# Optimization experiments

Hardware: AMD Instinct MI355X
Metric: run time of the kernel (lower is better)

Reference implementation:

```python
import jax, jax.numpy as jnp
import numpy as np

N_NODES = 50000
N_EDGES = 800000
D_IN = 128
HIDDEN = 128
N_CLASSES = 10
N_GRAPHS = 128


def setup_inputs() -> dict:
    key = jax.random.key(0)
    ks = jax.random.split(key, 16)
    x = jax.random.normal(ks[0], (N_NODES, D_IN), dtype=jnp.float32)
    edge_index = jax.random.randint(ks[1], (2, N_EDGES), 0, N_NODES, dtype=jnp.int64)
    batch = jnp.sort(jax.random.randint(ks[2], (N_NODES,), 0, N_GRAPHS, dtype=jnp.int64))

    def lin(k, fin, fout):
        return jax.random.normal(k, (fin, fout), dtype=jnp.float32) / np.sqrt(fin)

    inp = {"x": x, "edge_index": edge_index, "batch": batch}
    # SAGEConv layer 1: in=D_IN, out=HIDDEN; layers 2,3: HIDDEN->HIDDEN
    dims = [(D_IN, HIDDEN), (HIDDEN, HIDDEN), (HIDDEN, HIDDEN)]
    for i, (fin, fout) in enumerate(dims, start=1):
        inp[f"Wl{i}"] = lin(ks[2 + 2 * i], fin, fout)       # neighbor transform
        inp[f"bl{i}"] = jnp.zeros((fout,), dtype=jnp.float32)
        inp[f"Wr{i}"] = lin(ks[3 + 2 * i], fin, fout)       # root transform
    inp["W1"] = lin(ks[12], HIDDEN, HIDDEN)
    inp["b1"] = jnp.zeros((HIDDEN,), dtype=jnp.float32)
    inp["W2"] = lin(ks[13], HIDDEN, N_CLASSES)
    inp["b2"] = jnp.zeros((N_CLASSES,), dtype=jnp.float32)
    return inp


def _sage_conv(x, src, dst, Wl, bl, Wr):
    # mean-aggregate neighbor features then linear; plus root linear (PyG SAGEConv)
    msg = x[src]                                               # [E, d] gather
    agg = jax.ops.segment_sum(msg, dst, num_segments=N_NODES)  # [N, d]
    cnt = jax.ops.segment_sum(jnp.ones_like(dst, dtype=x.dtype), dst,
                              num_segments=N_NODES)
    agg = agg / jnp.maximum(cnt, 1.0)[:, None]
    return agg @ Wl + bl + x @ Wr


def reference(x, edge_index, batch, Wl1, bl1, Wr1, Wl2, bl2, Wr2,
              Wl3, bl3, Wr3, W1, b1, W2, b2):
    src, dst = edge_index[0], edge_index[1]
    h = jax.nn.relu(_sage_conv(x, src, dst, Wl1, bl1, Wr1))
    h = jax.nn.relu(_sage_conv(h, src, dst, Wl2, bl2, Wr2))
    h = jax.nn.relu(_sage_conv(h, src, dst, Wl3, bl3, Wr3))
    # global_mean_pool over graph ids
    gsum = jax.ops.segment_sum(h, batch, num_segments=N_GRAPHS)
    gcnt = jax.ops.segment_sum(jnp.ones((h.shape[0],), h.dtype), batch,
                               num_segments=N_GRAPHS)
    g = gsum / jnp.maximum(gcnt, 1.0)[:, None]                 # [G, hidden]
    g = jax.nn.relu(g @ W1 + b1)
    # dropout is identity at inference (training=False)
    logits = g @ W2 + b2
    return jax.nn.log_softmax(logits, axis=-1)
```

## Files before the change

### kernel.cpp

```cpp
#include <hip/hip_runtime.h>

#define NN 50000
#define NE 800000
#define D 128
#define NG 128
#define NGRP 8
#define GRPSZ 6250
#define FILL_NB 392
#define ESL ((NE + 48) / 49)
#define CAP 64

typedef __attribute__((ext_vector_type(8))) short bf16x8;
typedef __attribute__((ext_vector_type(4))) float f32x4;

static __device__ __forceinline__ ushort f2bf(float f) {
    uint x = __float_as_uint(f);
    x += 0x7fffu + ((x >> 16) & 1u);
    return (ushort)(x >> 16);
}
static __device__ __forceinline__ float bf2f(ushort u) { return __uint_as_float((uint)u << 16); }
static __device__ __forceinline__ float blo16(uint u) { return __uint_as_float(u << 16); }
static __device__ __forceinline__ float bhi16(uint u) { return __uint_as_float(u & 0xffff0000u); }

#define CASTX_NB 6250
#define CASTW_NB 192
__global__ __launch_bounds__(256) void fusedA_kernel(
    const float* __restrict__ x, ushort* __restrict__ xb,
    const float* __restrict__ Wl1, const float* __restrict__ Wr1,
    const float* __restrict__ Wl2, const float* __restrict__ Wr2,
    const float* __restrict__ Wl3, const float* __restrict__ Wr3,
    ushort* __restrict__ wlh, ushort* __restrict__ wll,
    ushort* __restrict__ wrh, ushort* __restrict__ wrl) {
    const int bid = blockIdx.x;
    if (bid < CASTX_NB) {
        int i = bid * 256 + threadIdx.x;
        int n = i >> 5, g = i & 31;
        float4 v = *reinterpret_cast<const float4*>(x + (size_t)n * D + g * 4);
        ushort4 o;
        o.x = f2bf(v.x); o.y = f2bf(v.y); o.z = f2bf(v.z); o.w = f2bf(v.w);
        *reinterpret_cast<ushort4*>(xb + (size_t)n * D + g * 4) = o;
    } else {
        int i = (bid - CASTX_NB) * 256 + threadIdx.x;
        int layer = i >> 14, j = i & 16383;
        int colg = j >> 7, k = j & 127;
        const float* Wl = (layer == 0) ? Wl1 : ((layer == 1) ? Wl2 : Wl3);
        const float* Wr = (layer == 0) ? Wr1 : ((layer == 1) ? Wr2 : Wr3);
        float vl = Wl[k * 128 + colg];
        float vr = Wr[k * 128 + colg];
        ushort hl = f2bf(vl), hr = f2bf(vr);
        wlh[i] = hl; wll[i] = f2bf(vl - bf2f(hl));
        wrh[i] = hr; wrl[i] = f2bf(vr - bf2f(hr));
    }
}

static __device__ __forceinline__ void gemm2_body(
    char* As, int rb,
    const ushort* __restrict__ ain,
    const ushort* __restrict__ wlh, const ushort* __restrict__ wll,
    const ushort* __restrict__ wrh, const ushort* __restrict__ wrl,
    const float* __restrict__ bl,
    ushort* __restrict__ y, ushort* __restrict__ z, int N) {
    const int tid = threadIdx.x;
    const int w = tid >> 6, lane = tid & 63;
    const int row0 = rb * 128;
    const int lrow = lane & 15, lk = lane >> 4;
    const int colg = w * 16 + lrow;

    bf16x8 ylh[4], yll[4], zrh[4], zrl[4];
#pragma unroll
    for (int kb = 0; kb < 4; ++kb) {
        int off = colg * 128 + kb * 32 + lk * 8;
        ylh[kb] = *reinterpret_cast<const bf16x8*>(wlh + off);
        yll[kb] = *reinterpret_cast<const bf16x8*>(wll + off);
        zrh[kb] = *reinterpret_cast<const bf16x8*>(wrh + off);
        zrl[kb] = *reinterpret_cast<const bf16x8*>(wrl + off);
    }
    const float bias = bl[colg];

    {
        const char* gbase = (const char*)ain + (size_t)row0 * 256;
#pragma unroll
        for (int i = 0; i < 4; ++i) {
            int Ld = i * 8192 + w * 1024 + lane * 16;
            int gs = Ld ^ (((Ld >> 8) & 7) << 4);
            __builtin_amdgcn_global_load_lds(
                (const uint*)(gbase + gs),
                (uint*)(As + i * 8192 + w * 1024), 16, 0, 0);
        }
    }
    __syncthreads();

#pragma unroll
    for (int mt = 0; mt < 8; ++mt) {
        const int ar = mt * 16 + lrow;
        const int swz = (ar & 7) << 4;
        const char* ap = As + ar * 256;
        bf16x8 ah[4];
#pragma unroll
        for (int kb = 0; kb < 4; ++kb) {
            int b_ = kb * 64 + lk * 16;
            ah[kb] = *reinterpret_cast<const bf16x8*>(ap + (b_ ^ swz));
        }
        f32x4 accy = {0.f, 0.f, 0.f, 0.f}, accz = {0.f, 0.f, 0.f, 0.f};
#pragma unroll
        for (int kb = 0; kb < 4; ++kb) {
            accy = __builtin_amdgcn_mfma_f32_16x16x32_bf16(ah[kb], ylh[kb], accy, 0, 0, 0);
            accy = __builtin_amdgcn_mfma_f32_16x16x32_bf16(ah[kb], yll[kb], accy, 0, 0, 0);
            accz = __builtin_amdgcn_mfma_f32_16x16x32_bf16(ah[kb], zrh[kb], accz, 0, 0, 0);
            accz = __builtin_amdgcn_mfma_f32_16x16x32_bf16(ah[kb], zrl[kb], accz, 0, 0, 0);
        }
#pragma unroll
        for (int r = 0; r < 4; ++r) {
            int rowg = row0 + mt * 16 + lk * 4 + r;
            if (rowg < N) {
                y[(size_t)rowg * D + colg] = f2bf(accy[r]);
                z[(size_t)rowg * D + colg] = f2bf(accz[r] + bias);
            }
        }
    }
}

__global__ __launch_bounds__(512, 4) void gemm2_kernel(
    const ushort* __restrict__ ain,
    const ushort* __restrict__ wlh, const ushort* __restrict__ wll,
    const ushort* __restrict__ wrh, const ushort* __restrict__ wrl,
    const float* __restrict__ bl,
    ushort* __restrict__ y, ushort* __restrict__ z, int N) {
    __shared__ char As[128 * 256];
    gemm2_body(As, blockIdx.x, ain, wlh, wll, wrh, wrl, bl, y, z, N);
}

#define GEMM_NB 391
__global__ __launch_bounds__(512, 4) void fusedB_kernel(
    const ushort* __restrict__ ain,
    const ushort* __restrict__ wlh, const ushort* __restrict__ wll,
    const ushort* __restrict__ wrh, const ushort* __restrict__ wrl,
    const float* __restrict__ bl,
    ushort* __restrict__ y, ushort* __restrict__ z,
    const int* __restrict__ src, const int* __restrict__ dst,
    int* __restrict__ fillp, int* __restrict__ col, int N) {
    __shared__ char As[128 * 256];
    const int bid = blockIdx.x;
    if (bid < FILL_NB) {
        const int grp = bid & 7;
        const int slice = bid >> 3;
        const int dlo = grp * GRPSZ, dhi = dlo + GRPSZ;
        const int e0 = slice * ESL;
        const int e1 = min(e0 + ESL, NE);
        for (int e = e0 + (int)threadIdx.x; e < e1; e += 512) {
            int d = dst[e];
            if (d >= dlo && d < dhi) {
                int s = src[e];
                int pos = atomicAdd(&fillp[d], 1);
                if (pos < CAP) col[d * CAP + pos] = s;
            }
        }
    } else {
        gemm2_body(As, bid - FILL_NB, ain, wlh, wll, wrh, wrl, bl, y, z, N);
    }
}

__global__ __launch_bounds__(256) void gather_relu(
    const ushort* __restrict__ y, ushort* __restrict__ z,
    const int* __restrict__ deg, const int* __restrict__ col, int N) {
    int wid = (blockIdx.x * 256 + threadIdx.x) >> 6;
    if (wid >= N) return;
    const int lane = threadIdx.x & 63;
    const int h = lane >> 5, li = lane & 31;
    const int dg = deg[wid];
    const int lo = wid * CAP;
    const int hi = lo + min(dg, CAP);
    float a0 = 0.f, a1 = 0.f, a2 = 0.f, a3 = 0.f;
    int e = lo + h;
    for (; e + 6 < hi; e += 8) {
        int s0 = col[e], s1 = col[e + 2], s2 = col[e + 4], s3 = col[e + 6];
        uint2 v0 = *reinterpret_cast<const uint2*>(y + (size_t)s0 * D + li * 4);
        uint2 v1 = *reinterpret_cast<const uint2*>(y + (size_t)s1 * D + li * 4);
        uint2 v2 = *reinterpret_cast<const uint2*>(y + (size_t)s2 * D + li * 4);
        uint2 v3 = *reinterpret_cast<const uint2*>(y + (size_t)s3 * D + li * 4);
        a0 += (blo16(v0.x) + blo16(v1.x)) + (blo16(v2.x) + blo16(v3.x));
        a1 += (bhi16(v0.x) + bhi16(v1.x)) + (bhi16(v2.x) + bhi16(v3.x));
        a2 += (blo16(v0.y) + blo16(v1.y)) + (blo16(v2.y) + blo16(v3.y));
        a3 += (bhi16(v0.y) + bhi16(v1.y)) + (bhi16(v2.y) + bhi16(v3.y));
    }
    for (; e < hi; e += 2) {
        uint2 v = *reinterpret_cast<const uint2*>(y + (size_t)col[e] * D + li * 4);
        a0 += blo16(v.x); a1 += bhi16(v.x);
        a2 += blo16(v.y); a3 += bhi16(v.y);
    }
    a0 += __shfl_xor(a0, 32, 64);
    a1 += __shfl_xor(a1, 32, 64);
    a2 += __shfl_xor(a2, 32, 64);
    a3 += __shfl_xor(a3, 32, 64);
    if (h == 0) {
        float inv = 1.0f / fmaxf((float)dg, 1.0f);
        uint2 zv = *reinterpret_cast<const uint2*>(z + (size_t)wid * D + li * 4);
        float h0 = fmaxf(a0 * inv + blo16(zv.x), 0.f);
        float h1 = fmaxf(a1 * inv + bhi16(zv.x), 0.f);
        float h2 = fmaxf(a2 * inv + blo16(zv.y), 0.f);
        float h3 = fmaxf(a3 * inv + bhi16(zv.y), 0.f);
        uint2 o;
        o.x = (uint)f2bf(h0) | ((uint)f2bf(h1) << 16);
        o.y = (uint)f2bf(h2) | ((uint)f2bf(h3) << 16);
        *reinterpret_cast<uint2*>(z + (size_t)wid * D + li * 4) = o;
    }
}

__global__ __launch_bounds__(256) void pool_head(
    const ushort* __restrict__ hbuf, const int* __restrict__ batch, int N,
    const float* __restrict__ W1, const float* __restrict__ b1,
    const float* __restrict__ W2, const float* __restrict__ b2,
    float* __restrict__ out) {
    __shared__ float part[4][128];
    __shared__ float gl[128];
    __shared__ float tl[128];
    __shared__ float lg[10];
    __shared__ float red[2];
    const int b = blockIdx.x;
    const int tid = threadIdx.x;
    const int wv = tid >> 6, lane = tid & 63;
    const int cb = lane * 2;

    int lo = 0, r = N;
    while (lo < r) { int m = (lo + r) >> 1; if (batch[m] < b) lo = m + 1; else r = m; }
    int hi = lo; r = N;
    while (hi < r) { int m = (hi + r) >> 1; if (batch[m] < b + 1) hi = m + 1; else r = m; }

    float a0 = 0.f, a1 = 0.f;
    for (int n = lo + wv; n < hi; n += 4) {
        uint v = *reinterpret_cast<const uint*>(hbuf + (size_t)n * D + cb);
        a0 += blo16(v); a1 += bhi16(v);
    }
    part[wv][cb] = a0;
    part[wv][cb + 1] = a1;
    __syncthreads();

    const int j = tid & 127;
    if (tid < 128) {
        float c = fmaxf((float)(hi - lo), 1.0f);
        gl[j] = (part[0][j] + part[1][j] + part[2][j] + part[3][j]) / c;
    }
    __syncthreads();

    if (tid < 128) {
        float t = b1[j];
        for (int k = 0; k < 128; ++k) t += gl[k] * W1[k * 128 + j];
        tl[j] = fmaxf(t, 0.0f);
    }
    __syncthreads();

    if (tid < 10) {
        float acc = b2[tid];
        for (int k = 0; k < 128; ++k) acc += tl[k] * W2[k * 10 + tid];
        lg[tid] = acc;
    }
    __syncthreads();

    if (tid == 0) {
        float m = lg[0];
        for (int q = 1; q < 10; ++q) m = fmaxf(m, lg[q]);
        float s = 0.0f;
        for (int q = 0; q < 10; ++q) s += expf(lg[q] - m);
        red[0] = m;
        red[1] = logf(s);
    }
    __syncthreads();

    if (tid < 10) out[b * 10 + tid] = lg[tid] - red[0] - red[1];
}

extern "C" void kernel_launch(void* const* d_in, const int* in_sizes, int n_in,
                              void* d_out, int out_size, void* d_ws, size_t ws_size,
                              hipStream_t stream) {
    const float* x    = (const float*)d_in[0];
    const int*   ei   = (const int*)d_in[1];
    const int*   src  = ei;
    const int*   dst  = ei + NE;
    const int*   batch = (const int*)d_in[2];
    const float* Wl1 = (const float*)d_in[3];
    const float* bl1 = (const float*)d_in[4];
    const float* Wr1 = (const float*)d_in[5];
    const float* Wl2 = (const float*)d_in[6];
    const float* bl2 = (const float*)d_in[7];
    const float* Wr2 = (const float*)d_in[8];
    const float* Wl3 = (const float*)d_in[9];
    const float* bl3 = (const float*)d_in[10];
    const float* Wr3 = (const float*)d_in[11];
    const float* W1  = (const float*)d_in[12];
    const float* b1  = (const float*)d_in[13];
    const float* W2  = (const float*)d_in[14];
    const float* b2  = (const float*)d_in[15];
    float* out = (float*)d_out;

    char* p = (char*)d_ws;
    char* S0 = p; p += 12800000;
    char* S1 = p; p += 12800000;
    char* S2 = p; p += 12800000;
    ushort* wlh = (ushort*)p; p += 3 * 32768;
    ushort* wll = (ushort*)p; p += 3 * 32768;
    ushort* wrh = (ushort*)p; p += 3 * 32768;
    ushort* wrl = (ushort*)p; p += 3 * 32768;
    int* fillp  = (int*)p;   p += 200000;
    int* colb   = (int*)p;   p += NN * CAP * 4;

    hipMemsetAsync(fillp, 0, (size_t)NN * 4, stream);

    fusedA_kernel<<<CASTX_NB + CASTW_NB, 256, 0, stream>>>(
        x, (ushort*)S0, Wl1, Wr1, Wl2, Wr2, Wl3, Wr3, wlh, wll, wrh, wrl);

    const int agg_blocks = (NN * 64 + 255) / 256;

    fusedB_kernel<<<FILL_NB + GEMM_NB, 512, 0, stream>>>(
        (ushort*)S0, wlh, wll, wrh, wrl, bl1, (ushort*)S1, (ushort*)S2,
        src, dst, fillp, colb, NN);

    gather_relu<<<agg_blocks, 256, 0, stream>>>((ushort*)S1, (ushort*)S2, fillp, colb, NN);
    gemm2_kernel<<<GEMM_NB, 512, 0, stream>>>((ushort*)S2, wlh + 16384, wll + 16384,
                                              wrh + 16384, wrl + 16384, bl2,
                                              (ushort*)S1, (ushort*)S0, NN);
    gather_relu<<<agg_blocks, 256, 0, stream>>>((ushort*)S1, (ushort*)S0, fillp, colb, NN);
    gemm2_kernel<<<GEMM_NB, 512, 0, stream>>>((ushort*)S0, wlh + 32768, wll + 32768,
                                              wrh + 32768, wrl + 32768, bl3,
                                              (ushort*)S1, (ushort*)S2, NN);
    gather_relu<<<agg_blocks, 256, 0, stream>>>((ushort*)S1, (ushort*)S2, fillp, colb, NN);

    pool_head<<<NG, 256, 0, stream>>>((ushort*)S2, batch, NN, W1, b1, W2, b2, out);
}
```

Measured before the change: 241.4 us.

## Split gather by node range and overlap with next layer GEMM; 16-bit column indices

The gather+ReLU pass is split into two node ranges. The upper half is fused into one launch with the next layer's GEMM over the lower row-blocks, whose inputs are already final, and the remaining GEMM blocks run afterward. This aims to overlap memory-bound gather with compute-bound GEMM and shorten the serial chain. A fourth scratch buffer avoids write conflicts. Column indices are also stored as ushort to halve CSR traffic, but node ids go up to 50000 and fit in 16 bits, so this is valid only because N < 65536.

```diff
diff --git a/kernel.cpp b/kernel.cpp
--- a/kernel.cpp
+++ b/kernel.cpp
@@ -9,6 +9,12 @@
 #define FILL_NB 392
 #define ESL ((NE + 48) / 49)
 #define CAP 64
+#define GEMM_NB 391
+#define LOB 196
+#define HIB 195
+#define NSPL (LOB * 128)
+#define GLO_NB ((NSPL + 3) / 4)
+#define GHI_NB ((NN - NSPL + 3) / 4)
 
 typedef __attribute__((ext_vector_type(8))) short bf16x8;
 typedef __attribute__((ext_vector_type(4))) float f32x4;
@@ -125,12 +131,64 @@
     const ushort* __restrict__ wlh, const ushort* __restrict__ wll,
     const ushort* __restrict__ wrh, const ushort* __restrict__ wrl,
     const float* __restrict__ bl,
-    ushort* __restrict__ y, ushort* __restrict__ z, int N) {
+    ushort* __restrict__ y, ushort* __restrict__ z, int rb0, int N) {
     __shared__ char As[128 * 256];
-    gemm2_body(As, blockIdx.x, ain, wlh, wll, wrh, wrl, bl, y, z, N);
-}
-
-#define GEMM_NB 391
+    gemm2_body(As, rb0 + blockIdx.x, ain, wlh, wll, wrh, wrl, bl, y, z, N);
+}
+
+static __device__ __forceinline__ void gather_wave(
+    const ushort* __restrict__ y, ushort* __restrict__ z,
+    const int* __restrict__ deg, const ushort* __restrict__ colu, int node, int N) {
+    if (node >= N) return;
+    const int lane = threadIdx.x & 63;
+    const int h = lane >> 5, li = lane & 31;
+    const int dg = deg[node];
+    const int lo = node * CAP;
+    const int hi = lo + min(dg, CAP);
+    float a0 = 0.f, a1 = 0.f, a2 = 0.f, a3 = 0.f;
+    int e = lo + h;
+    for (; e + 6 < hi; e += 8) {
+        int s0 = colu[e], s1 = colu[e + 2], s2 = colu[e + 4], s3 = colu[e + 6];
+        uint2 v0 = *reinterpret_cast<const uint2*>(y + (size_t)s0 * D + li * 4);
+        uint2 v1 = *reinterpret_cast<const uint2*>(y + (size_t)s1 * D + li * 4);
+        uint2 v2 = *reinterpret_cast<const uint2*>(y + (size_t)s2 * D + li * 4);
+        uint2 v3 = *reinterpret_cast<const uint2*>(y + (size_t)s3 * D + li * 4);
+        a0 += (blo16(v0.x) + blo16(v1.x)) + (blo16(v2.x) + blo16(v3.x));
+        a1 += (bhi16(v0.x) + bhi16(v1.x)) + (bhi16(v2.x) + bhi16(v3.x));
+        a2 += (blo16(v0.y) + blo16(v1.y)) + (blo16(v2.y) + blo16(v3.y));
+        a3 += (bhi16(v0.y) + bhi16(v1.y)) + (bhi16(v2.y) + bhi16(v3.y));
+    }
+    for (; e < hi; e += 2) {
+        int s = colu[e];
+        uint2 v = *reinterpret_cast<const uint2*>(y + (size_t)s * D + li * 4);
+        a0 += blo16(v.x); a1 += bhi16(v.x);
+        a2 += blo16(v.y); a3 += bhi16(v.y);
+    }
+    a0 += __shfl_xor(a0, 32, 64);
+    a1 += __shfl_xor(a1, 32, 64);
+    a2 += __shfl_xor(a2, 32, 64);
+    a3 += __shfl_xor(a3, 32, 64);
+    if (h == 0) {
+        float inv = 1.0f / fmaxf((float)dg, 1.0f);
+        uint2 zv = *reinterpret_cast<const uint2*>(z + (size_t)node * D + li * 4);
+        float h0 = fmaxf(a0 * inv + blo16(zv.x), 0.f);
+        float h1 = fmaxf(a1 * inv + bhi16(zv.x), 0.f);
+        float h2 = fmaxf(a2 * inv + blo16(zv.y), 0.f);
+        float h3 = fmaxf(a3 * inv + bhi16(zv.y), 0.f);
+        uint2 o;
+        o.x = (uint)f2bf(h0) | ((uint)f2bf(h1) << 16);
+        o.y = (uint)f2bf(h2) | ((uint)f2bf(h3) << 16);
+        *reinterpret_cast<uint2*>(z + (size_t)node * D + li * 4) = o;
+    }
+}
+
+__global__ __launch_bounds__(256) void gather_relu(
+    const ushort* __restrict__ y, ushort* __restrict__ z,
+    const int* __restrict__ deg, const ushort* __restrict__ colu, int n0, int n1) {
+    int node = n0 + ((blockIdx.x * 256 + threadIdx.x) >> 6);
+    gather_wave(y, z, deg, colu, node, n1);
+}
+
 __global__ __launch_bounds__(512, 4) void fusedB_kernel(
     const ushort* __restrict__ ain,
     const ushort* __restrict__ wlh, const ushort* __restrict__ wll,
@@ -138,7 +196,7 @@
     const float* __restrict__ bl,
     ushort* __restrict__ y, ushort* __restrict__ z,
     const int* __restrict__ src, const int* __restrict__ dst,
-    int* __restrict__ fillp, int* __restrict__ col, int N) {
+    int* __restrict__ fillp, ushort* __restrict__ colu, int N) {
     __shared__ char As[128 * 256];
     const int bid = blockIdx.x;
     if (bid < FILL_NB) {
@@ -152,7 +210,7 @@
             if (d >= dlo && d < dhi) {
                 int s = src[e];
                 int pos = atomicAdd(&fillp[d], 1);
-                if (pos < CAP) col[d * CAP + pos] = s;
+                if (pos < CAP) colu[d * CAP + pos] = (ushort)s;
             }
         }
     } else {
@@ -160,49 +218,21 @@
     }
 }
 
-__global__ __launch_bounds__(256) void gather_relu(
-    const ushort* __restrict__ y, ushort* __restrict__ z,
-    const int* __restrict__ deg, const int* __restrict__ col, int N) {
-    int wid = (blockIdx.x * 256 + threadIdx.x) >> 6;
-    if (wid >= N) return;
-    const int lane = threadIdx.x & 63;
-    const int h = lane >> 5, li = lane & 31;
-    const int dg = deg[wid];
-    const int lo = wid * CAP;
-    const int hi = lo + min(dg, CAP);
-    float a0 = 0.f, a1 = 0.f, a2 = 0.f, a3 = 0.f;
-    int e = lo + h;
-    for (; e + 6 < hi; e += 8) {
-        int s0 = col[e], s1 = col[e + 2], s2 = col[e + 4], s3 = col[e + 6];
-        uint2 v0 = *reinterpret_cast<const uint2*>(y + (size_t)s0 * D + li * 4);
-        uint2 v1 = *reinterpret_cast<const uint2*>(y + (size_t)s1 * D + li * 4);
-        uint2 v2 = *reinterpret_cast<const uint2*>(y + (size_t)s2 * D + li * 4);
-        uint2 v3 = *reinterpret_cast<const uint2*>(y + (size_t)s3 * D + li * 4);
-        a0 += (blo16(v0.x) + blo16(v1.x)) + (blo16(v2.x) + blo16(v3.x));
-        a1 += (bhi16(v0.x) + bhi16(v1.x)) + (bhi16(v2.x) + bhi16(v3.x));
-        a2 += (blo16(v0.y) + blo16(v1.y)) + (blo16(v2.y) + blo16(v3.y));
-        a3 += (bhi16(v0.y) + bhi16(v1.y)) + (bhi16(v2.y) + bhi16(v3.y));
-    }
-    for (; e < hi; e += 2) {
-        uint2 v = *reinterpret_cast<const uint2*>(y + (size_t)col[e] * D + li * 4);
-        a0 += blo16(v.x); a1 += bhi16(v.x);
-        a2 += blo16(v.y); a3 += bhi16(v.y);
-    }
-    a0 += __shfl_xor(a0, 32, 64);
-    a1 += __shfl_xor(a1, 32, 64);
-    a2 += __shfl_xor(a2, 32, 64);
-    a3 += __shfl_xor(a3, 32, 64);
-    if (h == 0) {
-        float inv = 1.0f / fmaxf((float)dg, 1.0f);
-        uint2 zv = *reinterpret_cast<const uint2*>(z + (size_t)wid * D + li * 4);
-        float h0 = fmaxf(a0 * inv + blo16(zv.x), 0.f);
-        float h1 = fmaxf(a1 * inv + bhi16(zv.x), 0.f);
-        float h2 = fmaxf(a2 * inv + blo16(zv.y), 0.f);
-        float h3 = fmaxf(a3 * inv + bhi16(zv.y), 0.f);
-        uint2 o;
-        o.x = (uint)f2bf(h0) | ((uint)f2bf(h1) << 16);
-        o.y = (uint)f2bf(h2) | ((uint)f2bf(h3) << 16);
-        *reinterpret_cast<uint2*>(z + (size_t)wid * D + li * 4) = o;
+__global__ __launch_bounds__(512, 4) void fusedC_kernel(
+    const ushort* __restrict__ yg, ushort* __restrict__ zg,
+    const int* __restrict__ deg, const ushort* __restrict__ colu, int gn0, int gn1, int ngb,
+    const ushort* __restrict__ ain,
+    const ushort* __restrict__ wlh, const ushort* __restrict__ wll,
+    const ushort* __restrict__ wrh, const ushort* __restrict__ wrl,
+    const float* __restrict__ bl,
+    ushort* __restrict__ yout, ushort* __restrict__ zout, int grb0, int N) {
+    __shared__ char As[128 * 256];
+    const int bid = blockIdx.x;
+    if (bid < ngb) {
+        int node = gn0 + bid * 8 + ((int)threadIdx.x >> 6);
+        gather_wave(yg, zg, deg, colu, node, gn1);
+    } else {
+        gemm2_body(As, grb0 + (bid - ngb), ain, wlh, wll, wrh, wrl, bl, yout, zout, N);
     }
 }
 
@@ -296,33 +326,46 @@
     char* S0 = p; p += 12800000;
     char* S1 = p; p += 12800000;
     char* S2 = p; p += 12800000;
+    char* S3 = p; p += 12800000;
     ushort* wlh = (ushort*)p; p += 3 * 32768;
     ushort* wll = (ushort*)p; p += 3 * 32768;
     ushort* wrh = (ushort*)p; p += 3 * 32768;
     ushort* wrl = (ushort*)p; p += 3 * 32768;
-    int* fillp  = (int*)p;   p += 200000;
-    int* colb   = (int*)p;   p += NN * CAP * 4;
+    int* fillp   = (int*)p;   p += 200000;
+    ushort* colu = (ushort*)p; p += NN * CAP * 2;
 
     hipMemsetAsync(fillp, 0, (size_t)NN * 4, stream);
 
     fusedA_kernel<<<CASTX_NB + CASTW_NB, 256, 0, stream>>>(
         x, (ushort*)S0, Wl1, Wr1, Wl2, Wr2, Wl3, Wr3, wlh, wll, wrh, wrl);
 
-    const int agg_blocks = (NN * 64 + 255) / 256;
-
     fusedB_kernel<<<FILL_NB + GEMM_NB, 512, 0, stream>>>(
         (ushort*)S0, wlh, wll, wrh, wrl, bl1, (ushort*)S1, (ushort*)S2,
-        src, dst, fillp, colb, NN);
-
-    gather_relu<<<agg_blocks, 256, 0, stream>>>((ushort*)S1, (ushort*)S2, fillp, colb, NN);
-    gemm2_kernel<<<GEMM_NB, 512, 0, stream>>>((ushort*)S2, wlh + 16384, wll + 16384,
-                                              wrh + 16384, wrl + 16384, bl2,
-                                              (ushort*)S1, (ushort*)S0, NN);
-    gather_relu<<<agg_blocks, 256, 0, stream>>>((ushort*)S1, (ushort*)S0, fillp, colb, NN);
-    gemm2_kernel<<<GEMM_NB, 512, 0, stream>>>((ushort*)S0, wlh + 32768, wll + 32768,
-                                              wrh + 32768, wrl + 32768, bl3,
-                                              (ushort*)S1, (ushort*)S2, NN);
-    gather_relu<<<agg_blocks, 256, 0, stream>>>((ushort*)S1, (ushort*)S2, fillp, colb, NN);
+        src, dst, fillp, colu, NN);
+
+    gather_relu<<<GLO_NB, 256, 0, stream>>>((ushort*)S1, (ushort*)S2, fillp, colu, 0, NSPL);
+    {
+        int ngb = (NN - NSPL + 7) / 8;
+        fusedC_kernel<<<ngb + LOB, 512, 0, stream>>>(
+            (ushort*)S1, (ushort*)S2, fillp, colu, NSPL, NN, ngb,
+            (ushort*)S2, wlh + 16384, wll + 16384, wrh + 16384, wrl + 16384, bl2,
+            (ushort*)S3, (ushort*)S0, 0, NN);
+    }
+    gemm2_kernel<<<HIB, 512, 0, stream>>>((ushort*)S2, wlh + 16384, wll + 16384,
+                                          wrh + 16384, wrl + 16384, bl2,
+                                          (ushort*)S3, (ushort*)S0, LOB, NN);
+    gather_relu<<<GLO_NB, 256, 0, stream>>>((ushort*)S3, (ushort*)S0, fillp, colu, 0, NSPL);
+    {
+        int ngb = (NN - NSPL + 7) / 8;
+        fusedC_kernel<<<ngb + LOB, 512, 0, stream>>>(
+            (ushort*)S3, (ushort*)S0, fillp, colu, NSPL, NN, ngb,
+            (ushort*)S0, wlh + 32768, wll + 32768, wrh + 32768, wrl + 32768, bl3,
+            (ushort*)S1, (ushort*)S2, 0, NN);
+    }
+    gemm2_kernel<<<HIB, 512, 0, stream>>>((ushort*)S0, wlh + 32768, wll + 32768,
+                                          wrh + 32768, wrl + 32768, bl3,
+                                          (ushort*)S1, (ushort*)S2, LOB, NN);
+    gather_relu<<<(NN + 3) / 4, 256, 0, stream>>>((ushort*)S1, (ushort*)S2, fillp, colu, 0, NN);
 
     pool_head<<<NG, 256, 0, stream>>>((ushort*)S2, batch, NN, W1, b1, W2, b2, out);
 }
```

New measurement: 280.4 us. 1.16x slower.
